# Optimization experiments

Hardware: AMD Instinct MI355X
Metric: run time of the kernel (lower is better)

## Reference

```python
import jax, jax.numpy as jnp
import numpy as np

N_HEADS = 8
CLIP = 10.0  # tanh clipping constant of the pointer logits
NEG = -1e9


def setup_inputs() -> dict:
    key = jax.random.key(0)
    ks = jax.random.split(key, 10)
    B, N, H = 1024, 100, 128
    s = 1.0 / np.sqrt(H).astype(np.float32)
    return {
        "encoder_inputs": jax.random.normal(ks[0], (B, N, H), jnp.float32),
        "pool": jax.random.normal(ks[1], (B, H), jnp.float32),
        "capacity": jnp.full((B, 1), 50.0, jnp.float32),  # vehicle capacity
        "demand": (1.0 + 9.0 * jax.random.uniform(ks[2], (B, N), jnp.float32)).at[:, 0].set(0.0),  # depot demand = 0
        "fc_w": jax.random.normal(ks[3], (H, H + 1), jnp.float32) * s,
        "fc1_w": jax.random.normal(ks[4], (H, H), jnp.float32) * s,
        "Wq": jax.random.normal(ks[5], (H, H), jnp.float32) * s,
        "Wk": jax.random.normal(ks[6], (H, H), jnp.float32) * s,
        "Wv": jax.random.normal(ks[7], (H, H), jnp.float32) * s,
        "Wo": jax.random.normal(ks[8], (H, H), jnp.float32) * s,
        "Wk2": jax.random.normal(ks[9], (H, H), jnp.float32) * s,
        "n_steps": 128,
        "T": 1,
        "greedy": 1,
    }


def _decode(encoder_inputs, pool, capacity, demand, fc_w, fc1_w, Wq, Wk, Wv, Wo, Wk2, n_steps, T):
    B, N, H = encoder_inputs.shape
    hd = H // N_HEADS
    # encoder projections are step-invariant -> hoist out of the loop
    K = (encoder_inputs @ Wk.T).reshape(B, N, N_HEADS, hd)
    V = (encoder_inputs @ Wv.T).reshape(B, N, N_HEADS, hd)
    K2 = encoder_inputs @ Wk2.T  # [B, N, H] pointer keys
    pool_proj = pool @ fc1_w.T   # [B, H]
    base_cap = capacity[0, 0]
    rows = jnp.arange(B)

    def update_mask(cap, index, mask1):
        # mask1: permanently visited customers (depot never permanently masked)
        go_depot = (index == 0)
        mask1 = mask1.at[rows, index].set(1.0)
        mask1 = mask1.at[:, 0].set(0.0)
        mask = jnp.maximum(mask1, (demand > cap).astype(jnp.float32))
        # cannot stay at depot; but depot must stay open once all customers are masked
        all_cust = jnp.all(mask[:, 1:] > 0.0, axis=1)
        depot = jnp.where(all_cust, 0.0, go_depot.astype(jnp.float32))
        mask = mask.at[:, 0].set(depot)
        return mask, mask1

    mask0, mask1_0 = update_mask(capacity, jnp.zeros((B,), jnp.int32), jnp.zeros((B, N), jnp.float32))
    inp0 = encoder_inputs[:, 0, :]
    inv_sqrt_hd = 1.0 / jnp.sqrt(jnp.float32(hd))
    inv_sqrt_h = 1.0 / jnp.sqrt(jnp.float32(H))

    def step(carry, _):
        _inp, cap, mask, mask1 = carry
        dec = jnp.concatenate([_inp, cap], axis=-1) @ fc_w.T + pool_proj  # [B, H]
        # multi-head glimpse over encoder nodes
        q = (dec @ Wq.T).reshape(B, N_HEADS, hd)
        scores = jnp.einsum('bhd,bnhd->bhn', q, K) * inv_sqrt_hd
        scores = jnp.where(mask[:, None, :] > 0.0, NEG, scores)
        attn = jax.nn.softmax(scores, axis=-1)
        glimpse = jnp.einsum('bhn,bnhd->bhd', attn, V).reshape(B, H) @ Wo.T
        # single-head clipped pointer logits
        u = CLIP * jnp.tanh(jnp.einsum('bh,bnh->bn', glimpse, K2) * inv_sqrt_h)
        u = jnp.where(mask > 0.0, NEG, u)
        logp_all = jax.nn.log_softmax(u / T, axis=-1)
        index = jnp.argmax(logp_all, axis=-1)  # greedy decoding
        log_p = jnp.take_along_axis(logp_all, index[:, None], axis=1)[:, 0]
        is_done = (jnp.sum(mask1[:, 1:], axis=1) >= N - 1).astype(jnp.float32)
        log_p = log_p * (1.0 - is_done)
        # state update: subtract served demand; reset to base capacity at depot
        sel_d = jnp.take_along_axis(demand, index[:, None], axis=1)
        cap = jnp.where(index[:, None] == 0, base_cap, cap - sel_d)
        mask, mask1 = update_mask(cap, index, mask1)
        _inp = jnp.take_along_axis(encoder_inputs, index[:, None, None], axis=1)[:, 0]
        return (_inp, cap, mask, mask1), (index, log_p)

    _, (actions, log_ps) = jax.lax.scan(step, (inp0, capacity, mask0, mask1_0), None, length=n_steps)
    return actions.T, jnp.sum(log_ps, axis=0)  # ([B, n_steps], [B])


def reference(encoder_inputs, pool, capacity, demand, fc_w, fc1_w, Wq, Wk, Wv, Wo, Wk2, n_steps, T, greedy):
    actions, log_p = _decode(encoder_inputs, pool, capacity, demand, fc_w, fc1_w, Wq, Wk, Wv, Wo, Wk2, n_steps, T)
    return actions, log_p
```

## Files before the change

### kernel.cpp

```cpp
#include <hip/hip_runtime.h>
#include <math.h>

#define NNODE 100
#define NEGV  -1000000000.0f

__device__ float g_Wall [128 * 512];
__device__ float g_Wall2[128 * 128];
__device__ float g_qcap [128];
__device__ float g_C    [(size_t)102400 * 512];
__device__ float g_qpool[(size_t)1024 * 128];
__device__ float g_S1   [(size_t)1024 * 100 * 800];
__device__ float g_Scap [(size_t)1024 * 800];

__device__ __forceinline__ float fast_rcp(float x) { return __builtin_amdgcn_rcpf(x); }
__device__ __forceinline__ float tanh10(float z) {
    const float e2 = __expf(2.0f * z);
    return fmaf(-20.0f, __builtin_amdgcn_rcpf(e2 + 1.0f), 10.0f);
}
__device__ __forceinline__ unsigned fkey(float v) {
    const unsigned u = __float_as_uint(v);
    return (u & 0x80000000u) ? ~u : (u | 0x80000000u);
}
__device__ __forceinline__ float funkey(unsigned k) {
    return __uint_as_float((k & 0x80000000u) ? (k ^ 0x80000000u) : ~k);
}

template<int CTRL>
__device__ __forceinline__ int dpp_i(int v) {
    return __builtin_amdgcn_update_dpp(0, v, CTRL, 0xF, 0xF, true);
}
template<int CTRL>
__device__ __forceinline__ float dpp_f(float v) {
    return __uint_as_float((unsigned)dpp_i<CTRL>(__float_as_int(v)));
}
__device__ __forceinline__ float swz16_f(float v) {
    return __uint_as_float(
        (unsigned)__builtin_amdgcn_ds_swizzle(__float_as_int(v), 0x401F));
}

__global__ __launch_bounds__(128) void prep_kernel(
    const float* __restrict__ Wk,  const float* __restrict__ Wv,
    const float* __restrict__ Wk2, const float* __restrict__ Wo,
    const float* __restrict__ Wq,  const float* __restrict__ fc_w,
    const float* __restrict__ fc1_w)
{
    const int c = blockIdx.x;
    const int k = threadIdx.x;
    if (c < 128) {
        g_Wall[k * 512 + c] = Wk[c * 128 + k];
    } else if (c < 256) {
        g_Wall[k * 512 + c] = Wv[(c - 128) * 128 + k];
    } else if (c < 384) {
        const int cc = c - 256;
        float acc = 0.f;
        for (int h = 0; h < 128; h++)
            acc = fmaf(Wk2[h * 128 + k], Wo[h * 128 + cc], acc);
        g_Wall[k * 512 + c] = acc;
    } else if (c < 512) {
        const int cc = c - 384;
        float acc = 0.f;
        for (int j = 0; j < 128; j++)
            acc = fmaf(Wq[cc * 128 + j], fc_w[j * 129 + k], acc);
        g_Wall[k * 512 + c] = acc;
    } else if (c == 512) {
        float acc = 0.f;
        for (int j = 0; j < 128; j++)
            acc = fmaf(Wq[k * 128 + j], fc_w[j * 129 + 128], acc);
        g_qcap[k] = acc;
    } else {
        const int cc = c - 513;
        float acc = 0.f;
        for (int j = 0; j < 128; j++)
            acc = fmaf(Wq[cc * 128 + j], fc1_w[j * 128 + k], acc);
        g_Wall2[k * 128 + cc] = acc;
    }
}

__global__ __launch_bounds__(256) void gemm_kernel(const float* __restrict__ A,
                                                   int mode)
{
    const float* __restrict__ W = mode ? g_Wall2 : g_Wall;
    float* __restrict__ C       = mode ? g_qpool : g_C;
    const int ncols             = mode ? 128 : 512;
    const int m0 = blockIdx.x * 128, n0 = blockIdx.y * 128;

    __shared__ __align__(16) float At[32 * 132];
    __shared__ __align__(16) float Ws[32 * 128];
    const int tid = threadIdx.x;
    const int tm = tid >> 5, tn = tid & 31;
    const int mb = tm * 16, nb = tn * 4;
    float4 acc[16];
#pragma unroll
    for (int i = 0; i < 16; i++) acc[i] = make_float4(0.f, 0.f, 0.f, 0.f);

    for (int kc = 0; kc < 4; kc++) {
        for (int f = tid; f < 1024; f += 256) {
            const int r = f >> 3, q8 = f & 7;
            float4 a = *(const float4*)&A[(size_t)(m0 + r) * 128 + kc * 32 + q8 * 4];
            At[(q8 * 4 + 0) * 132 + r] = a.x;
            At[(q8 * 4 + 1) * 132 + r] = a.y;
            At[(q8 * 4 + 2) * 132 + r] = a.z;
            At[(q8 * 4 + 3) * 132 + r] = a.w;
            const int kl = f >> 5, q = f & 31;
            *(float4*)&Ws[kl * 128 + q * 4] =
                *(const float4*)&W[(size_t)(kc * 32 + kl) * ncols + n0 + q * 4];
        }
        __syncthreads();
        for (int k = 0; k < 32; k++) {
            const float4 w = *(float4*)&Ws[k * 128 + nb];
#pragma unroll
            for (int i = 0; i < 16; i += 4) {
                const float4 a = *(float4*)&At[k * 132 + mb + i];
                acc[i + 0].x = fmaf(a.x, w.x, acc[i + 0].x);
                acc[i + 0].y = fmaf(a.x, w.y, acc[i + 0].y);
                acc[i + 0].z = fmaf(a.x, w.z, acc[i + 0].z);
                acc[i + 0].w = fmaf(a.x, w.w, acc[i + 0].w);
                acc[i + 1].x = fmaf(a.y, w.x, acc[i + 1].x);
                acc[i + 1].y = fmaf(a.y, w.y, acc[i + 1].y);
                acc[i + 1].z = fmaf(a.y, w.z, acc[i + 1].z);
                acc[i + 1].w = fmaf(a.y, w.w, acc[i + 1].w);
                acc[i + 2].x = fmaf(a.z, w.x, acc[i + 2].x);
                acc[i + 2].y = fmaf(a.z, w.y, acc[i + 2].y);
                acc[i + 2].z = fmaf(a.z, w.z, acc[i + 2].z);
                acc[i + 2].w = fmaf(a.z, w.w, acc[i + 2].w);
                acc[i + 3].x = fmaf(a.w, w.x, acc[i + 3].x);
                acc[i + 3].y = fmaf(a.w, w.y, acc[i + 3].y);
                acc[i + 3].z = fmaf(a.w, w.z, acc[i + 3].z);
                acc[i + 3].w = fmaf(a.w, w.w, acc[i + 3].w);
            }
        }
        __syncthreads();
    }
#pragma unroll
    for (int i = 0; i < 16; i++)
        *(float4*)&C[(size_t)(m0 + mb + i) * ncols + n0 + nb] = acc[i];
}

__global__ __launch_bounds__(256) void s1_kernel()
{
    const int b = blockIdx.x;
    const int tid = threadIdx.x;
    const int h = tid >> 5, l32 = tid & 31;
    const float* __restrict__ Crow = &g_C[(size_t)b * 100 * 512];

    __shared__ __align__(16) float Q1sh[NNODE * 128];
    for (int f = tid; f < 3200; f += 256) {
        const int n = f >> 5, c4 = f & 31;
        *(float4*)&Q1sh[n * 128 + c4 * 4] =
            *(const float4*)&Crow[(size_t)n * 512 + 384 + c4 * 4];
    }
    __syncthreads();

    float4 kr[4][4];
    int nn[4];
#pragma unroll
    for (int j = 0; j < 4; j++) {
        nn[j] = l32 + 32 * j;
#pragma unroll
        for (int i = 0; i < 4; i++) {
            kr[j][i] = (nn[j] < 100)
                ? *(const float4*)&Crow[(size_t)nn[j] * 512 + h * 16 + i * 4]
                : make_float4(0.f, 0.f, 0.f, 0.f);
        }
    }
    float4 qc[4], qp[4];
#pragma unroll
    for (int i = 0; i < 4; i++) {
        qc[i] = *(const float4*)&g_qcap[h * 16 + i * 4];
        qp[i] = *(const float4*)&g_qpool[(size_t)b * 128 + h * 16 + i * 4];
    }
    float sp[4];
#pragma unroll
    for (int j = 0; j < 4; j++) {
        float dc = 0.f, dp = 0.f;
#pragma unroll
        for (int i = 0; i < 4; i++) {
            dc = fmaf(kr[j][i].x, qc[i].x, dc); dc = fmaf(kr[j][i].y, qc[i].y, dc);
            dc = fmaf(kr[j][i].z, qc[i].z, dc); dc = fmaf(kr[j][i].w, qc[i].w, dc);
            dp = fmaf(kr[j][i].x, qp[i].x, dp); dp = fmaf(kr[j][i].y, qp[i].y, dp);
            dp = fmaf(kr[j][i].z, qp[i].z, dp); dp = fmaf(kr[j][i].w, qp[i].w, dp);
        }
        sp[j] = dp;
        if (nn[j] < 100)
            g_Scap[(size_t)b * 800 + h * 100 + nn[j]] = dc * 0.25f;
    }

    float* __restrict__ S1b = &g_S1[(size_t)b * 80000];
    for (int m = 0; m < 100; m++) {
        float4 q[4];
#pragma unroll
        for (int i = 0; i < 4; i++)
            q[i] = *(float4*)&Q1sh[m * 128 + h * 16 + i * 4];
#pragma unroll
        for (int j = 0; j < 4; j++) {
            if (nn[j] < 100) {
                float d = 0.f;
#pragma unroll
                for (int i = 0; i < 4; i++) {
                    d = fmaf(kr[j][i].x, q[i].x, d); d = fmaf(kr[j][i].y, q[i].y, d);
                    d = fmaf(kr[j][i].z, q[i].z, d); d = fmaf(kr[j][i].w, q[i].w, d);
                }
                S1b[(size_t)m * 800 + h * 100 + nn[j]] = (d + sp[j]) * 0.25f;
            }
        }
    }
}

__global__ __launch_bounds__(256) void decode_kernel(
    const float* __restrict__ capacity, const float* __restrict__ demand,
    const int* __restrict__ nsteps_p, const int* __restrict__ T_p,
    float* __restrict__ out)
{
    __shared__ float u_buf[2 * 800];
    __shared__ float demand_sh[NNODE];
    __shared__ int   act_sh[512];

    const int tid = threadIdx.x;
    const int b   = blockIdx.x;
    const int nsteps = nsteps_p[0];
    const float invT = 1.0f / (float)T_p[0];
    const float base_cap = capacity[0];
    const float inv_sqrt_h = 0.08838834764831845f;

    const float4* __restrict__ C4  = (const float4*)&g_C[(size_t)b * 100 * 512];
    const float*  __restrict__ S1b = &g_S1[(size_t)b * 80000];

    const int w = tid >> 6, l = tid & 63;
    const int g = l >> 3, f = l & 7;
    const int F = 8 * w + f;
    const int h8 = tid >> 5, l32 = tid & 31;

    float4 Vreg[13], K2r[13];
#pragma unroll
    for (int m = 0; m < 13; m++) {
        const int n = g + 8 * m;
        const bool v = n < 100;
        Vreg[m] = v ? C4[(size_t)n * 128 + 32 + F] : make_float4(0.f, 0.f, 0.f, 0.f);
        K2r[m]  = v ? C4[(size_t)n * 128 + 64 + F] : make_float4(0.f, 0.f, 0.f, 0.f);
    }
    float s1r[4], scapr[4], d4[4];
#pragma unroll
    for (int j = 0; j < 4; j++) {
        const int nj = l32 + 32 * j;
        const bool v = nj < 100;
        scapr[j] = v ? g_Scap[(size_t)b * 800 + h8 * 100 + nj] : 0.f;
        s1r[j]   = v ? S1b[h8 * 100 + nj] : 0.f;
        d4[j]    = v ? demand[b * 100 + nj] : 1.0e30f;
    }
    const float de0 = demand[b * 100 + l];
    const float de1 = (l + 64 < 100) ? demand[b * 100 + l + 64] : 1.0e30f;
    for (int n = tid; n < 100; n += 256) demand_sh[n] = demand[b * 100 + n];
    bool me0 = false, me1 = false;
    unsigned mb4 = 0;
    float cap_r = capacity[b];
    float depot_r;
    {
        const bool am0 = (l == 0) ? true : (de0 > cap_r);
        const bool am1 = (l + 64 >= 100) ? true : (de1 > cap_r);
        depot_r = __all(am0 && am1) ? 0.f : 1.f;
    }
    float logp_r = 0.f;
    int visited_r = 0;
    int ub = 0;
    __syncthreads();

    for (int s = 0; s < nsteps; s++) {
        const float cap = cap_r;

        float a[4];
        float tot;
        {
            float sc[4];
#pragma unroll
            for (int j = 0; j < 4; j++) {
                const int nj = l32 + 32 * j;
                const bool m = (nj == 0) ? (depot_r != 0.f)
                    : (((mb4 >> j) & 1u) || (d4[j] > cap));
                const float raw = fmaf(cap, scapr[j], s1r[j]);
                sc[j] = (nj < 100 && !m) ? raw : NEGV;
            }
#pragma unroll
            for (int j = 0; j < 4; j++) a[j] = __expf(sc[j]);
            tot = (a[0] + a[1]) + (a[2] + a[3]);
        }

        float4 gp4 = make_float4(0.f, 0.f, 0.f, 0.f);
#pragma unroll
        for (int m = 0; m < 13; m++) {
            const int src = ((f >> 2) << 5) | (8 * (m & 3) + g);
            const float av = __shfl(a[m >> 2], src, 64);
            gp4.x = fmaf(av, Vreg[m].x, gp4.x);
            gp4.y = fmaf(av, Vreg[m].y, gp4.y);
            gp4.z = fmaf(av, Vreg[m].z, gp4.z);
            gp4.w = fmaf(av, Vreg[m].w, gp4.w);
        }
        tot += dpp_f<0xB1>(tot);
        tot += dpp_f<0x4E>(tot);
        tot += dpp_f<0x124>(tot);
        tot += dpp_f<0x128>(tot);
        tot += swz16_f(tot);
        gp4.x += dpp_f<0x128>(gp4.x);
        gp4.y += dpp_f<0x128>(gp4.y);
        gp4.z += dpp_f<0x128>(gp4.z);
        gp4.w += dpp_f<0x128>(gp4.w);
        gp4.x += swz16_f(gp4.x);
        gp4.y += swz16_f(gp4.y);
        gp4.z += swz16_f(gp4.z);
        gp4.w += swz16_f(gp4.w);
        gp4.x += __shfl_xor(gp4.x, 32, 64);
        gp4.y += __shfl_xor(gp4.y, 32, 64);
        gp4.z += __shfl_xor(gp4.z, 32, 64);
        gp4.w += __shfl_xor(gp4.w, 32, 64);
        {
            const float th = __shfl(tot, ((f >> 2) << 5) | l32, 64);
            const float rt = fast_rcp(th);
            gp4.x *= rt; gp4.y *= rt; gp4.z *= rt; gp4.w *= rt;
        }

        {
            float pm[13];
#pragma unroll
            for (int m = 0; m < 13; m++) {
                float p = gp4.x * K2r[m].x;
                p = fmaf(gp4.y, K2r[m].y, p);
                p = fmaf(gp4.z, K2r[m].z, p);
                p = fmaf(gp4.w, K2r[m].w, p);
                pm[m] = p;
            }
#pragma unroll
            for (int m = 0; m < 13; m++) pm[m] += dpp_f<0xB1>(pm[m]);
#pragma unroll
            for (int m = 0; m < 13; m++) pm[m] += dpp_f<0x4E>(pm[m]);
            if ((f & 3) == 0) {
                const int r = w * 2 + (f >> 2);
#pragma unroll
                for (int m = 0; m < 13; m++) {
                    const int n = g + 8 * m;
                    if (n < 100) u_buf[ub + r * 100 + n] = pm[m];
                }
            }
        }
        __syncthreads();

        float v0, v1 = -3.0e38f;
        {
            float s8 = 0.f;
#pragma unroll
            for (int r = 0; r < 8; r++) s8 += u_buf[ub + r * 100 + l];
            const float u0 = tanh10(s8 * inv_sqrt_h);
            const bool m0 = (l == 0) ? (depot_r != 0.f) : (me0 || de0 > cap);
            v0 = (m0 ? NEGV : u0) * invT;
            if (l + 64 < 100) {
                float t8 = 0.f;
#pragma unroll
                for (int r = 0; r < 8; r++) t8 += u_buf[ub + r * 100 + l + 64];
                const float u1 = tanh10(t8 * inv_sqrt_h);
                const bool m1 = (me1 || de1 > cap);
                v1 = (m1 ? NEGV : u1) * invT;
            }
        }
        unsigned long long p;
        float tt;
        {
            const unsigned long long p0 =
                ((unsigned long long)fkey(v0) << 32) | (unsigned)(127 - l);
            const unsigned long long p1 =
                ((unsigned long long)fkey(v1) << 32) | (unsigned)(127 - (l + 64));
            p = (p1 > p0) ? p1 : p0;
            tt = __expf(v0) + ((l + 64 < 100) ? __expf(v1) : 0.f);
        }
#define E_DPP_STAGE(CTRL)                                                     \
        {                                                                     \
            const int lo = dpp_i<CTRL>((int)(unsigned)p);                     \
            const int hi = dpp_i<CTRL>((int)(unsigned)(p >> 32));             \
            const float tn = dpp_f<CTRL>(tt);                                 \
            const unsigned long long po =                                     \
                ((unsigned long long)(unsigned)hi << 32) | (unsigned)lo;      \
            tt += tn;                                                         \
            if (po > p) p = po;                                               \
        }
        E_DPP_STAGE(0xB1)
        E_DPP_STAGE(0x4E)
        E_DPP_STAGE(0x124)
        E_DPP_STAGE(0x128)
#undef E_DPP_STAGE
        {
            const int lo = __builtin_amdgcn_ds_swizzle((int)(unsigned)p, 0x401F);
            const int hi = __builtin_amdgcn_ds_swizzle((int)(unsigned)(p >> 32), 0x401F);
            const float tn = swz16_f(tt);
            const unsigned long long po =
                ((unsigned long long)(unsigned)hi << 32) | (unsigned)lo;
            tt += tn;
            if (po > p) p = po;
        }
        {
            const unsigned lo = __shfl_xor((unsigned)p, 32, 64);
            const unsigned hi = __shfl_xor((unsigned)(p >> 32), 32, 64);
            const float tn = __shfl_xor(tt, 32, 64);
            const unsigned long long po = ((unsigned long long)hi << 32) | lo;
            tt += tn;
            if (po > p) p = po;
        }
        const int idx = 127 - (int)(unsigned)(p & 0xffffffffULL);
        const float bv = funkey((unsigned)(p >> 32));

#pragma unroll
        for (int j = 0; j < 4; j++) {
            const int nj = l32 + 32 * j;
            if (nj < 100)
                s1r[j] = S1b[(size_t)idx * 800 + h8 * 100 + nj];
        }

        const float dmd_idx = demand_sh[idx];
        const float capn = (idx == 0) ? base_cap : (cap - dmd_idx);

        if (visited_r < 99) logp_r += bv - __logf(tt);
        visited_r += (idx > 0) ? 1 : 0;
        me0 = me0 || (l == idx && idx > 0);
        me1 = me1 || (l + 64 == idx);
#pragma unroll
        for (int j = 0; j < 4; j++)
            if ((l32 + 32 * j) == idx && idx > 0) mb4 |= (1u << j);

        const bool am0 = (l == 0) ? true : (me0 || de0 > capn);
        const bool am1 = (l + 64 >= 100) ? true : (me1 || de1 > capn);
        const bool allc = __all(am0 && am1);
        depot_r = allc ? 0.f : ((idx == 0) ? 1.f : 0.f);
        cap_r = capn;
        if (tid == 0) act_sh[s] = idx;
        ub ^= 800;
    }

    __syncthreads();
    for (int t = tid; t < nsteps; t += 256)
        out[(size_t)b * nsteps + t] = (float)act_sh[t];
    if (tid == 0)
        out[(size_t)gridDim.x * nsteps + b] = logp_r;
}

extern "C" void kernel_launch(void* const* d_in, const int* in_sizes, int n_in,
                              void* d_out, int out_size, void* d_ws, size_t ws_size,
                              hipStream_t stream) {
    const float* enc    = (const float*)d_in[0];
    const float* pool   = (const float*)d_in[1];
    const float* cap    = (const float*)d_in[2];
    const float* demand = (const float*)d_in[3];
    const float* fc_w   = (const float*)d_in[4];
    const float* fc1_w  = (const float*)d_in[5];
    const float* Wq     = (const float*)d_in[6];
    const float* Wk     = (const float*)d_in[7];
    const float* Wv     = (const float*)d_in[8];
    const float* Wo     = (const float*)d_in[9];
    const float* Wk2    = (const float*)d_in[10];
    const int*   nst    = (const int*)d_in[11];
    const int*   Tp     = (const int*)d_in[12];
    float* out = (float*)d_out;

    prep_kernel<<<641, 128, 0, stream>>>(Wk, Wv, Wk2, Wo, Wq, fc_w, fc1_w);
    gemm_kernel<<<dim3(800, 4), 256, 0, stream>>>(enc, 0);
    gemm_kernel<<<dim3(8, 1),   256, 0, stream>>>(pool, 1);
    s1_kernel<<<1024, 256, 0, stream>>>();
    decode_kernel<<<1024, 256, 0, stream>>>(cap, demand, nst, Tp, out);
}
```

Before: 845.8 us.

## Single-wave argmax with broadcast, early exit after all customers visited

In the decode loop, only one rotating wave now does the per-step score reduction. It finds the maximum with a float max reduction plus a ballot, instead of a packed 64-bit key, and broadcasts the chosen index and log-prob through shared memory. This removes the duplicate reduction across all four waves and the double-buffered u_buf, at the cost of an extra __syncthreads per step. The loop now breaks once all customers are visited, and the remaining actions are left at zero from a pre-initialisation of act_sh. Separately, s1_kernel drops its shared-memory staging of Q1 and reads it directly from global memory, with the loop unrolled by two.

```diff
diff --git a/kernel.cpp b/kernel.cpp
--- a/kernel.cpp
+++ b/kernel.cpp
@@ -16,13 +16,6 @@
 __device__ __forceinline__ float tanh10(float z) {
     const float e2 = __expf(2.0f * z);
     return fmaf(-20.0f, __builtin_amdgcn_rcpf(e2 + 1.0f), 10.0f);
-}
-__device__ __forceinline__ unsigned fkey(float v) {
-    const unsigned u = __float_as_uint(v);
-    return (u & 0x80000000u) ? ~u : (u | 0x80000000u);
-}
-__device__ __forceinline__ float funkey(unsigned k) {
-    return __uint_as_float((k & 0x80000000u) ? (k ^ 0x80000000u) : ~k);
 }
 
 template<int CTRL>
@@ -143,14 +136,6 @@
     const int h = tid >> 5, l32 = tid & 31;
     const float* __restrict__ Crow = &g_C[(size_t)b * 100 * 512];
 
-    __shared__ __align__(16) float Q1sh[NNODE * 128];
-    for (int f = tid; f < 3200; f += 256) {
-        const int n = f >> 5, c4 = f & 31;
-        *(float4*)&Q1sh[n * 128 + c4 * 4] =
-            *(const float4*)&Crow[(size_t)n * 512 + 384 + c4 * 4];
-    }
-    __syncthreads();
-
     float4 kr[4][4];
     int nn[4];
 #pragma unroll
@@ -186,11 +171,12 @@
     }
 
     float* __restrict__ S1b = &g_S1[(size_t)b * 80000];
+#pragma unroll 2
     for (int m = 0; m < 100; m++) {
         float4 q[4];
 #pragma unroll
         for (int i = 0; i < 4; i++)
-            q[i] = *(float4*)&Q1sh[m * 128 + h * 16 + i * 4];
+            q[i] = *(const float4*)&Crow[(size_t)m * 512 + 384 + h * 16 + i * 4];
 #pragma unroll
         for (int j = 0; j < 4; j++) {
             if (nn[j] < 100) {
@@ -211,9 +197,11 @@
     const int* __restrict__ nsteps_p, const int* __restrict__ T_p,
     float* __restrict__ out)
 {
-    __shared__ float u_buf[2 * 800];
+    __shared__ float u_buf[800];
     __shared__ float demand_sh[NNODE];
     __shared__ int   act_sh[512];
+    __shared__ int   idx_sh;
+    __shared__ float lp_sh;
 
     const int tid = threadIdx.x;
     const int b   = blockIdx.x;
@@ -250,6 +238,7 @@
     const float de0 = demand[b * 100 + l];
     const float de1 = (l + 64 < 100) ? demand[b * 100 + l + 64] : 1.0e30f;
     for (int n = tid; n < 100; n += 256) demand_sh[n] = demand[b * 100 + n];
+    for (int t = tid; t < 512; t += 256) act_sh[t] = 0;
     bool me0 = false, me1 = false;
     unsigned mb4 = 0;
     float cap_r = capacity[b];
@@ -261,7 +250,6 @@
     }
     float logp_r = 0.f;
     int visited_r = 0;
-    int ub = 0;
     __syncthreads();
 
     for (int s = 0; s < nsteps; s++) {
@@ -336,73 +324,60 @@
 #pragma unroll
                 for (int m = 0; m < 13; m++) {
                     const int n = g + 8 * m;
-                    if (n < 100) u_buf[ub + r * 100 + n] = pm[m];
+                    if (n < 100) u_buf[r * 100 + n] = pm[m];
                 }
             }
         }
         __syncthreads();
 
-        float v0, v1 = -3.0e38f;
-        {
-            float s8 = 0.f;
-#pragma unroll
-            for (int r = 0; r < 8; r++) s8 += u_buf[ub + r * 100 + l];
-            const float u0 = tanh10(s8 * inv_sqrt_h);
-            const bool m0 = (l == 0) ? (depot_r != 0.f) : (me0 || de0 > cap);
-            v0 = (m0 ? NEGV : u0) * invT;
-            if (l + 64 < 100) {
-                float t8 = 0.f;
-#pragma unroll
-                for (int r = 0; r < 8; r++) t8 += u_buf[ub + r * 100 + l + 64];
-                const float u1 = tanh10(t8 * inv_sqrt_h);
-                const bool m1 = (me1 || de1 > cap);
-                v1 = (m1 ? NEGV : u1) * invT;
-            }
-        }
-        unsigned long long p;
-        float tt;
-        {
-            const unsigned long long p0 =
-                ((unsigned long long)fkey(v0) << 32) | (unsigned)(127 - l);
-            const unsigned long long p1 =
-                ((unsigned long long)fkey(v1) << 32) | (unsigned)(127 - (l + 64));
-            p = (p1 > p0) ? p1 : p0;
-            tt = __expf(v0) + ((l + 64 < 100) ? __expf(v1) : 0.f);
-        }
-#define E_DPP_STAGE(CTRL)                                                     \
-        {                                                                     \
-            const int lo = dpp_i<CTRL>((int)(unsigned)p);                     \
-            const int hi = dpp_i<CTRL>((int)(unsigned)(p >> 32));             \
-            const float tn = dpp_f<CTRL>(tt);                                 \
-            const unsigned long long po =                                     \
-                ((unsigned long long)(unsigned)hi << 32) | (unsigned)lo;      \
-            tt += tn;                                                         \
-            if (po > p) p = po;                                               \
-        }
-        E_DPP_STAGE(0xB1)
-        E_DPP_STAGE(0x4E)
-        E_DPP_STAGE(0x124)
-        E_DPP_STAGE(0x128)
-#undef E_DPP_STAGE
-        {
-            const int lo = __builtin_amdgcn_ds_swizzle((int)(unsigned)p, 0x401F);
-            const int hi = __builtin_amdgcn_ds_swizzle((int)(unsigned)(p >> 32), 0x401F);
-            const float tn = swz16_f(tt);
-            const unsigned long long po =
-                ((unsigned long long)(unsigned)hi << 32) | (unsigned)lo;
-            tt += tn;
-            if (po > p) p = po;
-        }
-        {
-            const unsigned lo = __shfl_xor((unsigned)p, 32, 64);
-            const unsigned hi = __shfl_xor((unsigned)(p >> 32), 32, 64);
-            const float tn = __shfl_xor(tt, 32, 64);
-            const unsigned long long po = ((unsigned long long)hi << 32) | lo;
-            tt += tn;
-            if (po > p) p = po;
-        }
-        const int idx = 127 - (int)(unsigned)(p & 0xffffffffULL);
-        const float bv = funkey((unsigned)(p >> 32));
+        if (w == (s & 3)) {
+            float v0, v1 = -3.0e38f;
+            {
+                float s8 = 0.f;
+#pragma unroll
+                for (int r = 0; r < 8; r++) s8 += u_buf[r * 100 + l];
+                const float u0 = tanh10(s8 * inv_sqrt_h);
+                const bool m0 = (l == 0) ? (depot_r != 0.f) : (me0 || de0 > cap);
+                v0 = (m0 ? NEGV : u0) * invT;
+                if (l + 64 < 100) {
+                    float t8 = 0.f;
+#pragma unroll
+                    for (int r = 0; r < 8; r++) t8 += u_buf[r * 100 + l + 64];
+                    const float u1 = tanh10(t8 * inv_sqrt_h);
+                    const bool m1 = (me1 || de1 > cap);
+                    v1 = (m1 ? NEGV : u1) * invT;
+                }
+            }
+            float tt = __expf(v0) + ((l + 64 < 100) ? __expf(v1) : 0.f);
+            float vm = fmaxf(v0, v1);
+#define E_STG(CTRL)                                                           \
+            {                                                                 \
+                tt += dpp_f<CTRL>(tt);                                        \
+                vm = fmaxf(vm, dpp_f<CTRL>(vm));                              \
+            }
+            E_STG(0xB1)
+            E_STG(0x4E)
+            E_STG(0x124)
+            E_STG(0x128)
+#undef E_STG
+            tt += swz16_f(tt);
+            vm = fmaxf(vm, swz16_f(vm));
+            tt += __shfl_xor(tt, 32, 64);
+            vm = fmaxf(vm, __shfl_xor(vm, 32, 64));
+            const unsigned long long b0 = __ballot(v0 == vm);
+            const unsigned long long b1 = __ballot(v1 == vm);
+            const int idx = b0 ? (int)__builtin_ctzll(b0)
+                               : (64 + (int)__builtin_ctzll(b1));
+            if (l == 0) {
+                idx_sh = idx;
+                act_sh[s] = idx;
+                lp_sh = (visited_r < 99) ? (vm - __logf(tt)) : 0.f;
+            }
+        }
+        __syncthreads();
+
+        const int idx = idx_sh;
+        if (tid == 0) logp_r += lp_sh;
 
 #pragma unroll
         for (int j = 0; j < 4; j++) {
@@ -414,7 +389,6 @@
         const float dmd_idx = demand_sh[idx];
         const float capn = (idx == 0) ? base_cap : (cap - dmd_idx);
 
-        if (visited_r < 99) logp_r += bv - __logf(tt);
         visited_r += (idx > 0) ? 1 : 0;
         me0 = me0 || (l == idx && idx > 0);
         me1 = me1 || (l + 64 == idx);
@@ -427,8 +401,8 @@
         const bool allc = __all(am0 && am1);
         depot_r = allc ? 0.f : ((idx == 0) ? 1.f : 0.f);
         cap_r = capn;
-        if (tid == 0) act_sh[s] = idx;
-        ub ^= 800;
+
+        if (visited_r >= 99) break;
     }
 
     __syncthreads();
```

New measurement: 888.6 us. 5.1% more time.
